# Kernel optimization log

Hardware: AMD Instinct MI355X
Metric: run time of the kernel (lower is better)

The kernel has to match this reference:

```python
import jax, jax.numpy as jnp
import numpy as np


def _build_resonance(T):
    """res[i,j] = Omega(gcd(i+1, j+1)) = sum_p min(v_p(i+1), v_p(j+1))."""
    n = np.arange(1, T + 1)
    g = np.gcd.outer(n, n)  # [T,T], values in 1..T
    # smallest-prime-factor sieve up to T, then Omega (prime factors w/ multiplicity)
    spf = np.arange(T + 1)
    for i in range(2, int(T ** 0.5) + 1):
        if spf[i] == i:
            sl = spf[i * i:: i]
            np.minimum(sl, i, out=sl)
    omega = np.zeros(T + 1, np.int64)
    for m in range(2, T + 1):
        omega[m] = omega[m // spf[m]] + 1
    return omega[g].astype(np.float32)


def _build_buffers(T):
    res = _build_resonance(T)
    causal = np.tril(np.ones((T, T), np.float32))
    ident = np.eye(T, dtype=np.float32)
    allowed = ((res > 0) | (ident > 0)) & (causal > 0)  # bool [T,T]
    rbias = np.log1p(res) * allowed.astype(np.float32)
    return jnp.asarray(rbias), jnp.asarray(allowed)


def setup_inputs() -> dict:
    key = jax.random.key(0)
    B, T, C, H = 8, 2048, 1024, 64
    kx, kq, kk, kv = jax.random.split(key, 4)
    x = jax.random.normal(kx, (B, T, C), dtype=jnp.float32)
    scale = C ** -0.5
    Wq = jax.random.normal(kq, (C, H), dtype=jnp.float32) * scale
    Wk = jax.random.normal(kk, (C, H), dtype=jnp.float32) * scale
    Wv = jax.random.normal(kv, (C, H), dtype=jnp.float32) * scale
    rbias, allowed = _build_buffers(T)
    return {"x": x, "Wq": Wq, "Wk": Wk, "Wv": Wv, "rbias": rbias, "allowed": allowed}


def reference(x, Wq, Wk, Wv, rbias, allowed):
    B, T, C = x.shape
    q = x @ Wq  # [B,T,H]
    k = x @ Wk
    v = x @ Wv
    w = jnp.einsum("bth,bsh->bts", q, k) * (C ** -0.5)  # note: scaled by C, as in source
    w = w + rbias[:T, :T]
    w = jnp.where(allowed[:T, :T], w, -jnp.inf)
    a = jax.nn.softmax(w, axis=-1)  # every row has diagonal allowed -> no NaN
    return a @ v  # [B,T,H]
```

## Files before the change

kernel.cpp:

```cpp
#include <hip/hip_runtime.h>

#define T_SEQ 2048
#define NB    8
#define CDIM  1024
#define HDIM  64
#define PPB   80

typedef __attribute__((ext_vector_type(8))) short short8;
typedef __attribute__((ext_vector_type(4))) float float4v;

__device__ inline short f2bf(float x) {
    unsigned u = __builtin_bit_cast(unsigned int, x);
    u += 0x7FFFu + ((u >> 16) & 1u);
    return (short)(u >> 16);
}

__device__ inline void dma16(const void* g, void* l) {
    __builtin_amdgcn_global_load_lds(
        (const __attribute__((address_space(1))) unsigned int*)g,
        (__attribute__((address_space(3))) unsigned int*)l, 16, 0, 0);
}

__global__ __launch_bounds__(256) void wcvt_kernel(
    const float* __restrict__ Wq, const float* __restrict__ Wk,
    const float* __restrict__ Wv, short* __restrict__ Wbt)
{
    __shared__ float tile[64][65];
    const int w  = blockIdx.y;
    const int k0 = blockIdx.x * 64;
    const float* Ws[3] = {Wq, Wk, Wv};
    const float* W = Ws[w];
    const int n  = threadIdx.x & 63;
    const int kq = threadIdx.x >> 6;
#pragma unroll
    for (int i = 0; i < 16; ++i) {
        int kk = kq + i * 4;
        tile[kk][n] = W[(size_t)(k0 + kk) * HDIM + n];
    }
    __syncthreads();
    const int kk = threadIdx.x & 63;
#pragma unroll
    for (int i = 0; i < 16; ++i) {
        int nn = kq + i * 4;
        Wbt[((size_t)(w * HDIM + nn)) * CDIM + k0 + kk] = f2bf(tile[kk][nn]);
    }
}

__global__ __launch_bounds__(256) void proj_kernel(
    const float* __restrict__ x, const short* __restrict__ Wbt,
    short* __restrict__ qb, short* __restrict__ kb, short* __restrict__ vtb)
{
    __shared__ short As[2][32 * 64];
    __shared__ short Bs[2][192 * 64];

    const int tid  = threadIdx.x;
    const int wave = tid >> 6, lane = tid & 63;
    const int quad = lane >> 4, l16 = lane & 15;
    const int m0   = blockIdx.x * 32;
    const int arow = tid >> 3;
    const int achk = tid & 7;
    const int gchk = (achk ^ (arow & 7)) * 8;

    const float* xsrc = x + (size_t)(m0 + arow) * CDIM + achk * 8;

    float4v acc[2][3];
#pragma unroll
    for (int mt = 0; mt < 2; ++mt)
#pragma unroll
        for (int i = 0; i < 3; ++i) acc[mt][i] = (float4v){0.f, 0.f, 0.f, 0.f};

    {
        float4 a0 = *(const float4*)(xsrc);
        float4 a1 = *(const float4*)(xsrc + 4);
#pragma unroll
        for (int i = 0; i < 6; ++i)
            dma16(Wbt + (size_t)(i * 32 + arow) * CDIM + gchk,
                  &Bs[0][i * 2048 + tid * 8]);
        short8 s;
        s[0] = f2bf(a0.x); s[1] = f2bf(a0.y); s[2] = f2bf(a0.z); s[3] = f2bf(a0.w);
        s[4] = f2bf(a1.x); s[5] = f2bf(a1.y); s[6] = f2bf(a1.z); s[7] = f2bf(a1.w);
        *(short8*)&As[0][arow * 64 + gchk] = s;
    }

    int p = 0;
    for (int kt = 0; kt < 16; ++kt) {
        __syncthreads();
        const bool more = (kt + 1) < 16;
        float4 a0, a1;
        if (more) {
            const float* src = xsrc + (kt + 1) * 64;
            a0 = *(const float4*)(src);
            a1 = *(const float4*)(src + 4);
#pragma unroll
            for (int i = 0; i < 6; ++i)
                dma16(Wbt + (size_t)(i * 32 + arow) * CDIM + (kt + 1) * 64 + gchk,
                      &Bs[p ^ 1][i * 2048 + tid * 8]);
        }
#pragma unroll
        for (int ks = 0; ks < 2; ++ks) {
            short8 af[2];
#pragma unroll
            for (int mt = 0; mt < 2; ++mt)
                af[mt] = *(const short8*)&As[p][(mt * 16 + l16) * 64
                         + (((ks * 4 + quad) ^ (l16 & 7)) * 8)];
#pragma unroll
            for (int i = 0; i < 3; ++i) {
                const int ct = wave * 3 + i;
                short8 bf_ = *(const short8*)&Bs[p][(ct * 16 + l16) * 64
                             + (((ks * 4 + quad) ^ (l16 & 7)) * 8)];
#pragma unroll
                for (int mt = 0; mt < 2; ++mt)
                    acc[mt][i] = __builtin_amdgcn_mfma_f32_16x16x32_bf16(af[mt], bf_, acc[mt][i], 0, 0, 0);
            }
        }
        if (more) {
            short8 s;
            s[0] = f2bf(a0.x); s[1] = f2bf(a0.y); s[2] = f2bf(a0.z); s[3] = f2bf(a0.w);
            s[4] = f2bf(a1.x); s[5] = f2bf(a1.y); s[6] = f2bf(a1.z); s[7] = f2bf(a1.w);
            *(short8*)&As[p ^ 1][arow * 64 + gchk] = s;
        }
        p ^= 1;
    }

#pragma unroll
    for (int i = 0; i < 3; ++i) {
        const int ctg = wave * 3 + i;
        const int mat = ctg >> 2;
        const int n   = (ctg & 3) * 16 + l16;
#pragma unroll
        for (int mt = 0; mt < 2; ++mt)
#pragma unroll
            for (int r = 0; r < 4; ++r) {
                const int m = m0 + mt * 16 + quad * 4 + r;
                if (mat == 0)      qb[(size_t)m * HDIM + n] = f2bf(acc[mt][i][r] * 0.03125f);
                else if (mat == 1) kb[(size_t)m * HDIM + n] = f2bf(acc[mt][i][r]);
                else {
                    int bb = m >> 11, tt = m & (T_SEQ - 1);
                    vtb[((size_t)bb * HDIM + n) * T_SEQ + tt] = f2bf(acc[mt][i][r]);
                }
            }
    }
}

__global__ __launch_bounds__(256) void attn_part_kernel(
    const short* __restrict__ qb, const short* __restrict__ kb,
    const short* __restrict__ vtb, const float* __restrict__ rbias,
    float* __restrict__ Op, float2* __restrict__ mlp)
{
    __shared__ short Ks[2][64 * 64];
    __shared__ short Vs[2][64 * 64];
    __shared__ short Ps[4][16][72];

    const int b   = blockIdx.y;
    const int tid = threadIdx.x;
    const int wave = tid >> 6, lane = tid & 63;
    const int quad = lane >> 4, l16 = lane & 15;
    const int srow = tid >> 3;
    const int gchk = ((tid & 7) ^ (srow & 7)) * 8;

    int qt64 = 0, c = blockIdx.x, cum = 0;
    while (true) { int ch = (qt64 + 8) >> 3; if (c < ch) break; c -= ch; cum += ch; ++qt64; }
    const int j0 = c * 8;
    const int j1 = (j0 + 8 < qt64 + 1) ? j0 + 8 : qt64 + 1;
    const int qrow0 = qt64 * 64 + wave * 16;

    const short* qptr = qb + (size_t)(b * T_SEQ + qrow0 + l16) * HDIM;
    short8 qf0 = *(const short8*)(qptr + quad * 8);
    short8 qf1 = *(const short8*)(qptr + 32 + quad * 8);

    float4v oacc[4];
#pragma unroll
    for (int i = 0; i < 4; ++i) oacc[i] = (float4v){0.f, 0.f, 0.f, 0.f};
    float m_run[4] = {-1e30f, -1e30f, -1e30f, -1e30f};
    float l_run[4] = {0.f, 0.f, 0.f, 0.f};

    {
        const int s0 = j0 * 64;
#pragma unroll
        for (int i = 0; i < 2; ++i) {
            dma16(kb + (size_t)(b * T_SEQ + s0 + i * 32 + srow) * HDIM + gchk,
                  &Ks[0][i * 2048 + tid * 8]);
            dma16(vtb + (size_t)(b * HDIM + i * 32 + srow) * T_SEQ + s0 + gchk,
                  &Vs[0][i * 2048 + tid * 8]);
        }
    }

    int p = 0;
    for (int j = j0; j < j1; ++j) {
        __syncthreads();
        if (j + 1 < j1) {
            const int sn = (j + 1) * 64;
#pragma unroll
            for (int i = 0; i < 2; ++i) {
                dma16(kb + (size_t)(b * T_SEQ + sn + i * 32 + srow) * HDIM + gchk,
                      &Ks[p ^ 1][i * 2048 + tid * 8]);
                dma16(vtb + (size_t)(b * HDIM + i * 32 + srow) * T_SEQ + sn + gchk,
                      &Vs[p ^ 1][i * 2048 + tid * 8]);
            }
        }
        const int s0 = j * 64;

        float rbv[4][4];
#pragma unroll
        for (int nt = 0; nt < 4; ++nt) {
            int s_idx = s0 + nt * 16 + l16;
#pragma unroll
            for (int r = 0; r < 4; ++r)
                rbv[nt][r] = rbias[(size_t)(qrow0 + quad * 4 + r) * T_SEQ + s_idx];
        }

        float4v sa[4];
#pragma unroll
        for (int nt = 0; nt < 4; ++nt) {
            const int rbase = (nt * 16 + l16) * 64;
            short8 kf0 = *(const short8*)&Ks[p][rbase + ((quad ^ (l16 & 7)) * 8)];
            short8 kf1 = *(const short8*)&Ks[p][rbase + (((4 + quad) ^ (l16 & 7)) * 8)];
            float4v a = {0.f, 0.f, 0.f, 0.f};
            a = __builtin_amdgcn_mfma_f32_16x16x32_bf16(qf0, kf0, a, 0, 0, 0);
            a = __builtin_amdgcn_mfma_f32_16x16x32_bf16(qf1, kf1, a, 0, 0, 0);
            sa[nt] = a;
        }

        float pm[4][4];
        float mt[4] = {-1e30f, -1e30f, -1e30f, -1e30f};
#pragma unroll
        for (int nt = 0; nt < 4; ++nt) {
            int s_idx = s0 + nt * 16 + l16;
#pragma unroll
            for (int r = 0; r < 4; ++r) {
                int t_idx = qrow0 + quad * 4 + r;
                float rb = rbv[nt][r];
                bool ok = (rb > 0.f) || ((t_idx == 0) && (s_idx == 0));
                float sv = ok ? (sa[nt][r] + rb) : -1e30f;
                pm[nt][r] = sv;
                mt[r] = fmaxf(mt[r], sv);
            }
        }
#pragma unroll
        for (int off = 1; off < 16; off <<= 1)
#pragma unroll
            for (int r = 0; r < 4; ++r)
                mt[r] = fmaxf(mt[r], __shfl_xor(mt[r], off, 64));
        float alpha[4];
#pragma unroll
        for (int r = 0; r < 4; ++r) {
            float mn = fmaxf(m_run[r], mt[r]);
            alpha[r] = __expf(m_run[r] - mn);
            m_run[r] = mn;
        }
        float rs[4] = {0.f, 0.f, 0.f, 0.f};
#pragma unroll
        for (int nt = 0; nt < 4; ++nt)
#pragma unroll
            for (int r = 0; r < 4; ++r) {
                float pv = (pm[nt][r] > -1e29f) ? __expf(pm[nt][r] - m_run[r]) : 0.f;
                pm[nt][r] = pv;
                rs[r] += pv;
            }
#pragma unroll
        for (int off = 1; off < 16; off <<= 1)
#pragma unroll
            for (int r = 0; r < 4; ++r)
                rs[r] += __shfl_xor(rs[r], off, 64);
#pragma unroll
        for (int r = 0; r < 4; ++r) {
            l_run[r] = l_run[r] * alpha[r] + rs[r];
            oacc[0][r] *= alpha[r]; oacc[1][r] *= alpha[r];
            oacc[2][r] *= alpha[r]; oacc[3][r] *= alpha[r];
        }

#pragma unroll
        for (int nt = 0; nt < 4; ++nt)
#pragma unroll
            for (int r = 0; r < 4; ++r)
                Ps[wave][quad * 4 + r][nt * 16 + l16] = f2bf(pm[nt][r]);

#pragma unroll
        for (int ks = 0; ks < 2; ++ks) {
            short8 pf = *(const short8*)&Ps[wave][l16][ks * 32 + quad * 8];
#pragma unroll
            for (int ht = 0; ht < 4; ++ht) {
                short8 vf = *(const short8*)&Vs[p][(ht * 16 + l16) * 64
                            + (((ks * 4 + quad) ^ (l16 & 7)) * 8)];
                oacc[ht] = __builtin_amdgcn_mfma_f32_16x16x32_bf16(pf, vf, oacc[ht], 0, 0, 0);
            }
        }
        p ^= 1;
    }

    const int pidx = b * PPB + cum + c;
    float* obase = Op + (size_t)pidx * 4096;
#pragma unroll
    for (int ht = 0; ht < 4; ++ht)
#pragma unroll
        for (int r = 0; r < 4; ++r)
            obase[(wave * 16 + quad * 4 + r) * 64 + ht * 16 + l16] = oacc[ht][r];
    if (l16 == 0)
#pragma unroll
        for (int r = 0; r < 4; ++r)
            mlp[(size_t)pidx * 64 + wave * 16 + quad * 4 + r] = make_float2(m_run[r], l_run[r]);
}

__global__ __launch_bounds__(256) void attn_merge_kernel(
    const float* __restrict__ Op, const float2* __restrict__ mlp,
    float* __restrict__ out)
{
    const int qt16 = blockIdx.x;
    const int b    = blockIdx.y;
    const int qt64 = qt16 >> 2;
    const int nch  = (qt64 + 8) >> 3;
    const int g8   = qt64 >> 3, rem = qt64 & 7;
    const int cum  = 4 * g8 * (g8 + 1) + rem * (g8 + 1);
    const int pbase = b * PPB + cum;

    const int row = threadIdx.x >> 4;
    const int c4  = (threadIdx.x & 15) * 4;
    const int prow = (qt16 & 3) * 16 + row;

    float2 ml[4];
    float4 o4[4];
#pragma unroll
    for (int cc = 0; cc < 4; ++cc) {
        ml[cc] = mlp[(size_t)(pbase + cc) * 64 + prow];
        o4[cc] = *(const float4*)&Op[(size_t)(pbase + cc) * 4096 + prow * 64 + c4];
        if (cc >= nch) ml[cc].x = -1e30f;
    }
    float M = -1e30f;
#pragma unroll
    for (int cc = 0; cc < 4; ++cc) M = fmaxf(M, ml[cc].x);
    float L = 0.f;
    float4 O = make_float4(0.f, 0.f, 0.f, 0.f);
#pragma unroll
    for (int cc = 0; cc < 4; ++cc) {
        float w = __expf(ml[cc].x - M);
        L += ml[cc].y * w;
        O.x += o4[cc].x * w; O.y += o4[cc].y * w;
        O.z += o4[cc].z * w; O.w += o4[cc].w * w;
    }
    float inv = 1.0f / L;
    float4 res = make_float4(O.x * inv, O.y * inv, O.z * inv, O.w * inv);
    *(float4*)&out[((size_t)(b * T_SEQ) + qt16 * 16 + row) * HDIM + c4] = res;
}

extern "C" void kernel_launch(void* const* d_in, const int* in_sizes, int n_in,
                              void* d_out, int out_size, void* d_ws, size_t ws_size,
                              hipStream_t stream) {
    (void)in_sizes; (void)n_in; (void)out_size; (void)ws_size;
    const float* x     = (const float*)d_in[0];
    const float* Wq    = (const float*)d_in[1];
    const float* Wk    = (const float*)d_in[2];
    const float* Wv    = (const float*)d_in[3];
    const float* rbias = (const float*)d_in[4];
    float* out = (float*)d_out;

    char* wsb   = (char*)d_ws;
    short* qb   = (short*)(wsb);
    short* kb   = (short*)(wsb + (size_t)2 * 1024 * 1024);
    short* vtb  = (short*)(wsb + (size_t)4 * 1024 * 1024);
    short* Wbt  = (short*)(wsb + (size_t)6 * 1024 * 1024);
    float* Op   = (float*)(wsb + (size_t)7 * 1024 * 1024);
    float2* mlp = (float2*)(wsb + (size_t)18 * 1024 * 1024);

    wcvt_kernel<<<dim3(16, 3), 256, 0, stream>>>(Wq, Wk, Wv, Wbt);
    proj_kernel<<<dim3(512), 256, 0, stream>>>(x, Wbt, qb, kb, vtb);
    attn_part_kernel<<<dim3(PPB, NB), 256, 0, stream>>>(qb, kb, vtb, rbias, Op, mlp);
    attn_merge_kernel<<<dim3(128, NB), 256, 0, stream>>>(Op, mlp, out);
}
```

Baseline: 172.0 us.

## Widen projection blocks, use DPP row reductions, reverse attention block order

The projection kernel now runs 512 threads per block, giving each of eight waves one M-tile instead of two, with narrower x loads and adjusted staging. The attention kernel replaces shuffle-based 16-lane max/sum reductions with DPP row operations, issues the rbias loads before the next K/V prefetch, and processes blocks in reverse order so the longest causal rows start first. Together these aim to raise latency hiding in the projection and shorten reduction and tail-scheduling costs in attention, at the risk of higher register pressure and more block-level synchronisation per K step.

```diff
diff --git a/kernel.cpp b/kernel.cpp
--- a/kernel.cpp
+++ b/kernel.cpp
@@ -7,6 +7,7 @@
 #define PPB   80
 
 typedef __attribute__((ext_vector_type(8))) short short8;
+typedef __attribute__((ext_vector_type(4))) short short4v;
 typedef __attribute__((ext_vector_type(4))) float float4v;
 
 __device__ inline short f2bf(float x) {
@@ -19,6 +20,21 @@
     __builtin_amdgcn_global_load_lds(
         (const __attribute__((address_space(1))) unsigned int*)g,
         (__attribute__((address_space(3))) unsigned int*)l, 16, 0, 0);
+}
+
+template<int CTRL> __device__ inline float dppf(float v) {
+    return __builtin_bit_cast(float,
+        __builtin_amdgcn_update_dpp(0, __builtin_bit_cast(int, v), CTRL, 0xF, 0xF, true));
+}
+__device__ inline float rowmax16(float v) {
+    v = fmaxf(v, dppf<0xB1>(v));  v = fmaxf(v, dppf<0x4E>(v));
+    v = fmaxf(v, dppf<0x141>(v)); v = fmaxf(v, dppf<0x140>(v));
+    return v;
+}
+__device__ inline float rowsum16(float v) {
+    v += dppf<0xB1>(v);  v += dppf<0x4E>(v);
+    v += dppf<0x141>(v); v += dppf<0x140>(v);
+    return v;
 }
 
 __global__ __launch_bounds__(256) void wcvt_kernel(
@@ -46,7 +62,7 @@
     }
 }
 
-__global__ __launch_bounds__(256) void proj_kernel(
+__global__ __launch_bounds__(512) void proj_kernel(
     const float* __restrict__ x, const short* __restrict__ Wbt,
     short* __restrict__ qb, short* __restrict__ kb, short* __restrict__ vtb)
 {
@@ -56,89 +72,77 @@
     const int tid  = threadIdx.x;
     const int wave = tid >> 6, lane = tid & 63;
     const int quad = lane >> 4, l16 = lane & 15;
+    const int mt   = wave >> 2;
+    const int cg   = wave & 3;
     const int m0   = blockIdx.x * 32;
-    const int arow = tid >> 3;
-    const int achk = tid & 7;
-    const int gchk = (achk ^ (arow & 7)) * 8;
-
-    const float* xsrc = x + (size_t)(m0 + arow) * CDIM + achk * 8;
-
-    float4v acc[2][3];
-#pragma unroll
-    for (int mt = 0; mt < 2; ++mt)
-#pragma unroll
-        for (int i = 0; i < 3; ++i) acc[mt][i] = (float4v){0.f, 0.f, 0.f, 0.f};
+
+    const int arow = tid >> 4;
+    const int ac   = tid & 15;
+    const int asw  = (((ac >> 1) ^ (arow & 7)) * 8) + (ac & 1) * 4;
+    const float* xsrc = x + (size_t)(m0 + arow) * CDIM + ac * 4;
+
+    const int brow = tid >> 3;
+    const int bsw  = ((tid & 7) ^ (brow & 7)) * 8;
+
+    float4v acc[3];
+#pragma unroll
+    for (int i = 0; i < 3; ++i) acc[i] = (float4v){0.f, 0.f, 0.f, 0.f};
 
     {
-        float4 a0 = *(const float4*)(xsrc);
-        float4 a1 = *(const float4*)(xsrc + 4);
-#pragma unroll
-        for (int i = 0; i < 6; ++i)
-            dma16(Wbt + (size_t)(i * 32 + arow) * CDIM + gchk,
-                  &Bs[0][i * 2048 + tid * 8]);
-        short8 s;
-        s[0] = f2bf(a0.x); s[1] = f2bf(a0.y); s[2] = f2bf(a0.z); s[3] = f2bf(a0.w);
-        s[4] = f2bf(a1.x); s[5] = f2bf(a1.y); s[6] = f2bf(a1.z); s[7] = f2bf(a1.w);
-        *(short8*)&As[0][arow * 64 + gchk] = s;
+        float4 a = *(const float4*)xsrc;
+#pragma unroll
+        for (int i = 0; i < 3; ++i)
+            dma16(Wbt + (size_t)(i * 64 + brow) * CDIM + bsw,
+                  &Bs[0][i * 4096 + tid * 8]);
+        short4v s; s[0]=f2bf(a.x); s[1]=f2bf(a.y); s[2]=f2bf(a.z); s[3]=f2bf(a.w);
+        *(short4v*)&As[0][arow * 64 + asw] = s;
     }
 
     int p = 0;
     for (int kt = 0; kt < 16; ++kt) {
         __syncthreads();
         const bool more = (kt + 1) < 16;
-        float4 a0, a1;
+        float4 a;
         if (more) {
-            const float* src = xsrc + (kt + 1) * 64;
-            a0 = *(const float4*)(src);
-            a1 = *(const float4*)(src + 4);
-#pragma unroll
-            for (int i = 0; i < 6; ++i)
-                dma16(Wbt + (size_t)(i * 32 + arow) * CDIM + (kt + 1) * 64 + gchk,
-                      &Bs[p ^ 1][i * 2048 + tid * 8]);
+            a = *(const float4*)(xsrc + (kt + 1) * 64);
+#pragma unroll
+            for (int i = 0; i < 3; ++i)
+                dma16(Wbt + (size_t)(i * 64 + brow) * CDIM + (kt + 1) * 64 + bsw,
+                      &Bs[p ^ 1][i * 4096 + tid * 8]);
         }
 #pragma unroll
         for (int ks = 0; ks < 2; ++ks) {
-            short8 af[2];
-#pragma unroll
-            for (int mt = 0; mt < 2; ++mt)
-                af[mt] = *(const short8*)&As[p][(mt * 16 + l16) * 64
-                         + (((ks * 4 + quad) ^ (l16 & 7)) * 8)];
+            const int cs = ((ks * 4 + quad) ^ (l16 & 7)) * 8;
+            short8 af = *(const short8*)&As[p][(mt * 16 + l16) * 64 + cs];
 #pragma unroll
             for (int i = 0; i < 3; ++i) {
-                const int ct = wave * 3 + i;
-                short8 bf_ = *(const short8*)&Bs[p][(ct * 16 + l16) * 64
-                             + (((ks * 4 + quad) ^ (l16 & 7)) * 8)];
-#pragma unroll
-                for (int mt = 0; mt < 2; ++mt)
-                    acc[mt][i] = __builtin_amdgcn_mfma_f32_16x16x32_bf16(af[mt], bf_, acc[mt][i], 0, 0, 0);
+                const int ct = cg * 3 + i;
+                short8 bf_ = *(const short8*)&Bs[p][(ct * 16 + l16) * 64 + cs];
+                acc[i] = __builtin_amdgcn_mfma_f32_16x16x32_bf16(af, bf_, acc[i], 0, 0, 0);
             }
         }
         if (more) {
-            short8 s;
-            s[0] = f2bf(a0.x); s[1] = f2bf(a0.y); s[2] = f2bf(a0.z); s[3] = f2bf(a0.w);
-            s[4] = f2bf(a1.x); s[5] = f2bf(a1.y); s[6] = f2bf(a1.z); s[7] = f2bf(a1.w);
-            *(short8*)&As[p ^ 1][arow * 64 + gchk] = s;
+            short4v s; s[0]=f2bf(a.x); s[1]=f2bf(a.y); s[2]=f2bf(a.z); s[3]=f2bf(a.w);
+            *(short4v*)&As[p ^ 1][arow * 64 + asw] = s;
         }
         p ^= 1;
     }
 
 #pragma unroll
     for (int i = 0; i < 3; ++i) {
-        const int ctg = wave * 3 + i;
+        const int ctg = cg * 3 + i;
         const int mat = ctg >> 2;
         const int n   = (ctg & 3) * 16 + l16;
 #pragma unroll
-        for (int mt = 0; mt < 2; ++mt)
-#pragma unroll
-            for (int r = 0; r < 4; ++r) {
-                const int m = m0 + mt * 16 + quad * 4 + r;
-                if (mat == 0)      qb[(size_t)m * HDIM + n] = f2bf(acc[mt][i][r] * 0.03125f);
-                else if (mat == 1) kb[(size_t)m * HDIM + n] = f2bf(acc[mt][i][r]);
-                else {
-                    int bb = m >> 11, tt = m & (T_SEQ - 1);
-                    vtb[((size_t)bb * HDIM + n) * T_SEQ + tt] = f2bf(acc[mt][i][r]);
-                }
-            }
+        for (int r = 0; r < 4; ++r) {
+            const int m = m0 + mt * 16 + quad * 4 + r;
+            if (mat == 0)      qb[(size_t)m * HDIM + n] = f2bf(acc[i][r] * 0.03125f);
+            else if (mat == 1) kb[(size_t)m * HDIM + n] = f2bf(acc[i][r]);
+            else {
+                int bb = m >> 11, tt = m & (T_SEQ - 1);
+                vtb[((size_t)bb * HDIM + n) * T_SEQ + tt] = f2bf(acc[i][r]);
+            }
+        }
     }
 }
 
@@ -155,10 +159,12 @@
     const int tid = threadIdx.x;
     const int wave = tid >> 6, lane = tid & 63;
     const int quad = lane >> 4, l16 = lane & 15;
+    const int swz  = l16 & 7;
     const int srow = tid >> 3;
     const int gchk = ((tid & 7) ^ (srow & 7)) * 8;
 
-    int qt64 = 0, c = blockIdx.x, cum = 0;
+    const int bx = (int)(gridDim.x - 1 - blockIdx.x);
+    int qt64 = 0, c = bx, cum = 0;
     while (true) { int ch = (qt64 + 8) >> 3; if (c < ch) break; c -= ch; cum += ch; ++qt64; }
     const int j0 = c * 8;
     const int j1 = (j0 + 8 < qt64 + 1) ? j0 + 8 : qt64 + 1;
@@ -188,6 +194,17 @@
     int p = 0;
     for (int j = j0; j < j1; ++j) {
         __syncthreads();
+        const int s0 = j * 64;
+
+        float rbv[4][4];
+#pragma unroll
+        for (int nt = 0; nt < 4; ++nt) {
+            int s_idx = s0 + nt * 16 + l16;
+#pragma unroll
+            for (int r = 0; r < 4; ++r)
+                rbv[nt][r] = rbias[(size_t)(qrow0 + quad * 4 + r) * T_SEQ + s_idx];
+        }
+
         if (j + 1 < j1) {
             const int sn = (j + 1) * 64;
 #pragma unroll
@@ -198,23 +215,13 @@
                       &Vs[p ^ 1][i * 2048 + tid * 8]);
             }
         }
-        const int s0 = j * 64;
-
-        float rbv[4][4];
-#pragma unroll
-        for (int nt = 0; nt < 4; ++nt) {
-            int s_idx = s0 + nt * 16 + l16;
-#pragma unroll
-            for (int r = 0; r < 4; ++r)
-                rbv[nt][r] = rbias[(size_t)(qrow0 + quad * 4 + r) * T_SEQ + s_idx];
-        }
 
         float4v sa[4];
 #pragma unroll
         for (int nt = 0; nt < 4; ++nt) {
             const int rbase = (nt * 16 + l16) * 64;
-            short8 kf0 = *(const short8*)&Ks[p][rbase + ((quad ^ (l16 & 7)) * 8)];
-            short8 kf1 = *(const short8*)&Ks[p][rbase + (((4 + quad) ^ (l16 & 7)) * 8)];
+            short8 kf0 = *(const short8*)&Ks[p][rbase + ((quad ^ swz) * 8)];
+            short8 kf1 = *(const short8*)&Ks[p][rbase + (((4 + quad) ^ swz) * 8)];
             float4v a = {0.f, 0.f, 0.f, 0.f};
             a = __builtin_amdgcn_mfma_f32_16x16x32_bf16(qf0, kf0, a, 0, 0, 0);
             a = __builtin_amdgcn_mfma_f32_16x16x32_bf16(qf1, kf1, a, 0, 0, 0);
@@ -236,15 +243,10 @@
                 mt[r] = fmaxf(mt[r], sv);
             }
         }
-#pragma unroll
-        for (int off = 1; off < 16; off <<= 1)
-#pragma unroll
-            for (int r = 0; r < 4; ++r)
-                mt[r] = fmaxf(mt[r], __shfl_xor(mt[r], off, 64));
         float alpha[4];
 #pragma unroll
         for (int r = 0; r < 4; ++r) {
-            float mn = fmaxf(m_run[r], mt[r]);
+            float mn = fmaxf(m_run[r], rowmax16(mt[r]));
             alpha[r] = __expf(m_run[r] - mn);
             m_run[r] = mn;
         }
@@ -258,13 +260,8 @@
                 rs[r] += pv;
             }
 #pragma unroll
-        for (int off = 1; off < 16; off <<= 1)
-#pragma unroll
-            for (int r = 0; r < 4; ++r)
-                rs[r] += __shfl_xor(rs[r], off, 64);
-#pragma unroll
         for (int r = 0; r < 4; ++r) {
-            l_run[r] = l_run[r] * alpha[r] + rs[r];
+            l_run[r] = l_run[r] * alpha[r] + rowsum16(rs[r]);
             oacc[0][r] *= alpha[r]; oacc[1][r] *= alpha[r];
             oacc[2][r] *= alpha[r]; oacc[3][r] *= alpha[r];
         }
@@ -281,7 +278,7 @@
 #pragma unroll
             for (int ht = 0; ht < 4; ++ht) {
                 short8 vf = *(const short8*)&Vs[p][(ht * 16 + l16) * 64
-                            + (((ks * 4 + quad) ^ (l16 & 7)) * 8)];
+                            + (((ks * 4 + quad) ^ swz) * 8)];
                 oacc[ht] = __builtin_amdgcn_mfma_f32_16x16x32_bf16(pf, vf, oacc[ht], 0, 0, 0);
             }
         }
@@ -362,7 +359,7 @@
     float2* mlp = (float2*)(wsb + (size_t)18 * 1024 * 1024);
 
     wcvt_kernel<<<dim3(16, 3), 256, 0, stream>>>(Wq, Wk, Wv, Wbt);
-    proj_kernel<<<dim3(512), 256, 0, stream>>>(x, Wbt, qb, kb, vtb);
+    proj_kernel<<<dim3(512), 512, 0, stream>>>(x, Wbt, qb, kb, vtb);
     attn_part_kernel<<<dim3(PPB, NB), 256, 0, stream>>>(qb, kb, vtb, rbias, Op, mlp);
     attn_merge_kernel<<<dim3(128, NB), 256, 0, stream>>>(Op, mlp, out);
 }
```

Result: no change. 170.4 us (-0.9%).
